# Performance work log

Measured on AMD Instinct MI355X. Metric: run time of the kernel, lower is better.

Reference implementation:

```python
import jax, jax.numpy as jnp
import numpy as np

TOP_K_PERCENT = 0.7


def setup_inputs() -> dict:
    key = jax.random.key(0)
    k1, k2, k3, k4 = jax.random.split(key, 4)
    B, C, H, W = 4, 19, 512, 1024
    logits = jax.random.normal(k1, (B, C, H, W), dtype=jnp.float32)
    labels = jax.random.randint(k2, (B, H, W), 0, C, dtype=jnp.int64)
    smooth_labels = jax.random.uniform(k3, (B, C, H, W), dtype=jnp.float32)
    weight2 = jax.random.uniform(k4, (C,), dtype=jnp.float32)
    return {"logits": logits, "labels": labels, "smooth_labels": smooth_labels, "weight2": weight2}


def reference(logits, labels, smooth_labels, weight2):
    # Fused equivalent of the per-class loop:
    #   cum[b,h,w] = sum_c smooth[b,c,h,w] * weight2[c] * (-log_softmax(logits)[b,c,h,w])
    # (ignore_label=-1 never matches any class index, so no masking occurs.)
    logp = jax.nn.log_softmax(logits, axis=1)  # [B,C,H,W]
    w = weight2[None, :, None, None]
    pixel_losses_2 = -(smooth_labels * w * logp).sum(axis=1)  # [B,H,W]
    flat = pixel_losses_2.reshape(-1)
    k = int(TOP_K_PERCENT * flat.shape[0])  # static shape -> python int
    top_vals, _ = jax.lax.top_k(flat, k)
    return top_vals.mean()
```

## Files before the change

kernel.cpp:

```cpp
#include <hip/hip_runtime.h>

#define NPIX 2097152
#define NT4  524288
#define NCH  19
#define CPL4 131072
#define KSEL 1468006u
#define LBS  1024
#define LBLK (NT4/LBS)
#define HB   512
#define NCP  8
#define H1B  4096
#define H2B  1024

#define OFF_COMB1 (NPIX*4)
#define OFF_COMB2 (OFF_COMB1 + NCP*H1B*4)
#define OFF_COMB3 (OFF_COMB2 + NCP*H2B*4)
#define OFF_TICK  (OFF_COMB3 + NCP*H2B*4)
#define OFF_PART  (OFF_TICK + 16)
#define OFF_CTRL  (OFF_PART + HB*8)
#define ZBYTES    (OFF_TICK + 16 - OFF_COMB1)

__global__ __launch_bounds__(LBS) void k_loss(
    const float* __restrict__ logits, const float* __restrict__ smooth,
    const float* __restrict__ wgt, float* __restrict__ loss,
    unsigned* __restrict__ comb1)
{
    __shared__ unsigned h[H1B];
    for (int j = threadIdx.x; j < H1B; j += LBS) h[j] = 0u;

    int tid = blockIdx.x * LBS + threadIdx.x;
    int img = tid >> 17;
    int rem = tid & (CPL4 - 1);
    const float4* L = (const float4*)logits + (size_t)img * (NCH * CPL4) + rem;
    const float4* S = (const float4*)smooth + (size_t)img * (NCH * CPL4) + rem;

    float4 xb[3], sb[3];
    #pragma unroll
    for (int i = 0; i < 3; ++i) {
        xb[i] = L[(size_t)i * CPL4];
        sb[i] = S[(size_t)i * CPL4];
    }
    __syncthreads();

    float s0 = 0.f, s1 = 0.f, s2 = 0.f, s3 = 0.f;
    float sw0 = 0.f, sw1 = 0.f, sw2 = 0.f, sw3 = 0.f;
    float swl0 = 0.f, swl1 = 0.f, swl2 = 0.f, swl3 = 0.f;

    #pragma unroll
    for (int c = 0; c < NCH; ++c) {
        float4 xv = xb[c % 3];
        float4 sv = sb[c % 3];
        if (c + 3 < NCH) {
            xb[c % 3] = L[(size_t)(c + 3) * CPL4];
            sb[c % 3] = S[(size_t)(c + 3) * CPL4];
        }
        float wc = wgt[c];
        s0 += __expf(xv.x); s1 += __expf(xv.y);
        s2 += __expf(xv.z); s3 += __expf(xv.w);
        float t0 = sv.x * wc, t1 = sv.y * wc, t2 = sv.z * wc, t3 = sv.w * wc;
        sw0 += t0; sw1 += t1; sw2 += t2; sw3 += t3;
        swl0 = fmaf(t0, xv.x, swl0); swl1 = fmaf(t1, xv.y, swl1);
        swl2 = fmaf(t2, xv.z, swl2); swl3 = fmaf(t3, xv.w, swl3);
    }

    float l0 = fmaxf(__logf(s0) * sw0 - swl0, 0.f);
    float l1 = fmaxf(__logf(s1) * sw1 - swl1, 0.f);
    float l2 = fmaxf(__logf(s2) * sw2 - swl2, 0.f);
    float l3 = fmaxf(__logf(s3) * sw3 - swl3, 0.f);
    ((float4*)loss)[tid] = make_float4(l0, l1, l2, l3);

    atomicAdd(&h[__float_as_uint(l0) >> 20], 1u);
    atomicAdd(&h[__float_as_uint(l1) >> 20], 1u);
    atomicAdd(&h[__float_as_uint(l2) >> 20], 1u);
    atomicAdd(&h[__float_as_uint(l3) >> 20], 1u);
    __syncthreads();

    unsigned* dst = comb1 + (size_t)(blockIdx.x & (NCP - 1)) * H1B;
    for (int j = threadIdx.x; j < H1B; j += LBS) {
        unsigned c = h[j];
        if (c) atomicAdd(&dst[j], c);
    }
}

__device__ __forceinline__ void suffix_select(
    unsigned* h, unsigned* cs, unsigned* shv, int cpt, unsigned need)
{
    int t = threadIdx.x;
    unsigned sum = 0;
    for (int j = 0; j < cpt; ++j) sum += h[t * cpt + j];
    cs[t] = sum;
    __syncthreads();
    for (int off = 1; off < 256; off <<= 1) {
        unsigned v = (t + off < 256) ? cs[t + off] : 0u;
        __syncthreads();
        cs[t] += v;
        __syncthreads();
    }
    unsigned St = cs[t], Sn = (t < 255) ? cs[t + 1] : 0u;
    if (St >= need && Sn < need) { shv[0] = (unsigned)t; shv[1] = Sn; }
    __syncthreads();
    if (t == 0) {
        unsigned cum = shv[1];
        for (int bb = (int)shv[0] * cpt + cpt - 1;; --bb) {
            unsigned c = h[bb];
            if (cum + c >= need) { shv[2] = (unsigned)bb; shv[3] = need - cum; break; }
            cum += c;
        }
    }
    __syncthreads();
}

#define ALD(p)  __hip_atomic_load((p), __ATOMIC_RELAXED, __HIP_MEMORY_SCOPE_AGENT)

__global__ __launch_bounds__(256) void k_h2(
    const uint4* __restrict__ lb, const unsigned* __restrict__ comb1,
    unsigned* __restrict__ comb2, unsigned* __restrict__ ctrl)
{
    __shared__ unsigned bins[H1B];
    __shared__ unsigned cs[256];
    __shared__ unsigned shv[4];
    int t = threadIdx.x, b = blockIdx.x;

    for (int j = t; j < H1B; j += 256) {
        unsigned s = 0;
        #pragma unroll
        for (int cp = 0; cp < NCP; ++cp) s += comb1[(size_t)cp * H1B + j];
        bins[j] = s;
    }
    __syncthreads();
    suffix_select(bins, cs, shv, H1B / 256, KSEL);
    unsigned p1 = shv[2], n1 = shv[3];
    if (b == 0 && t == 0) { ctrl[0] = p1; ctrl[1] = n1; }

    for (int j = t; j < H2B; j += 256) bins[j] = 0u;
    __syncthreads();
    int base = b * 256 + t;
    #pragma unroll
    for (int k = 0; k < NT4 / (HB * 256); ++k) {
        uint4 v = lb[(size_t)k * (HB * 256) + base];
        if ((v.x >> 20) == p1) atomicAdd(&bins[(v.x >> 10) & 1023u], 1u);
        if ((v.y >> 20) == p1) atomicAdd(&bins[(v.y >> 10) & 1023u], 1u);
        if ((v.z >> 20) == p1) atomicAdd(&bins[(v.z >> 10) & 1023u], 1u);
        if ((v.w >> 20) == p1) atomicAdd(&bins[(v.w >> 10) & 1023u], 1u);
    }
    __syncthreads();
    unsigned* dst = comb2 + (size_t)(b & (NCP - 1)) * H2B;
    for (int j = t; j < H2B; j += 256)
        if (bins[j]) atomicAdd(&dst[j], bins[j]);
}

__global__ __launch_bounds__(256) void k_h3(
    const uint4* __restrict__ lb, const unsigned* __restrict__ comb2,
    unsigned* __restrict__ comb3, double* __restrict__ partials,
    const unsigned* __restrict__ ctrl, unsigned* __restrict__ ticket,
    float* __restrict__ out)
{
    __shared__ unsigned bins[H2B];
    __shared__ unsigned cs[256];
    __shared__ unsigned shv[4];
    __shared__ double wsum[4];
    __shared__ unsigned sh_last;
    int t = threadIdx.x, b = blockIdx.x;
    unsigned p1 = ctrl[0], n1 = ctrl[1];

    for (int j = t; j < H2B; j += 256) {
        unsigned s = 0;
        #pragma unroll
        for (int cp = 0; cp < NCP; ++cp) s += comb2[(size_t)cp * H2B + j];
        bins[j] = s;
    }
    __syncthreads();
    suffix_select(bins, cs, shv, H2B / 256, n1);
    unsigned p2 = (p1 << 10) | shv[2], n2 = shv[3];

    for (int j = t; j < H2B; j += 256) bins[j] = 0u;
    __syncthreads();
    double acc = 0.0;
    int base = b * 256 + t;
    #pragma unroll
    for (int k = 0; k < NT4 / (HB * 256); ++k) {
        uint4 v = lb[(size_t)k * (HB * 256) + base];
        unsigned px = v.x >> 10, py = v.y >> 10, pz = v.z >> 10, pw = v.w >> 10;
        if (px == p2) atomicAdd(&bins[v.x & 1023u], 1u);
        else if (px > p2) acc += (double)__uint_as_float(v.x);
        if (py == p2) atomicAdd(&bins[v.y & 1023u], 1u);
        else if (py > p2) acc += (double)__uint_as_float(v.y);
        if (pz == p2) atomicAdd(&bins[v.z & 1023u], 1u);
        else if (pz > p2) acc += (double)__uint_as_float(v.z);
        if (pw == p2) atomicAdd(&bins[v.w & 1023u], 1u);
        else if (pw > p2) acc += (double)__uint_as_float(v.w);
    }
    __syncthreads();
    unsigned* dst = comb3 + (size_t)(b & (NCP - 1)) * H2B;
    for (int j = t; j < H2B; j += 256)
        if (bins[j]) atomicAdd(&dst[j], bins[j]);

    #pragma unroll
    for (int off = 32; off > 0; off >>= 1) acc += __shfl_down(acc, off, 64);
    if ((t & 63) == 0) wsum[t >> 6] = acc;
    __syncthreads();
    if (t == 0) {
        partials[b] = wsum[0] + wsum[1] + wsum[2] + wsum[3];
        __threadfence();
        sh_last = (atomicAdd(ticket, 1u) == HB - 1) ? 1u : 0u;
    }
    __syncthreads();
    if (!sh_last) return;

    __threadfence();
    for (int j = t; j < H2B; j += 256) {
        unsigned s = 0;
        #pragma unroll
        for (int cp = 0; cp < NCP; ++cp) s += ALD(&comb3[(size_t)cp * H2B + j]);
        bins[j] = s;
    }
    __syncthreads();
    suffix_select(bins, cs, shv, H2B / 256, n2);
    unsigned b3 = shv[2], r2 = shv[3];

    double a2 = __hip_atomic_load(&partials[t], __ATOMIC_RELAXED, __HIP_MEMORY_SCOPE_AGENT)
              + __hip_atomic_load(&partials[t + 256], __ATOMIC_RELAXED, __HIP_MEMORY_SCOPE_AGENT);
    #pragma unroll
    for (int kk = 0; kk < 4; ++kk) {
        int bb = t * 4 + kk;
        if (bb > (int)b3 && bins[bb])
            a2 += (double)bins[bb] * (double)__uint_as_float((p2 << 10) | (unsigned)bb);
    }
    #pragma unroll
    for (int off = 32; off > 0; off >>= 1) a2 += __shfl_down(a2, off, 64);
    if ((t & 63) == 0) wsum[t >> 6] = a2;
    __syncthreads();
    if (t == 0) {
        double tot = wsum[0] + wsum[1] + wsum[2] + wsum[3];
        tot += (double)r2 * (double)__uint_as_float((p2 << 10) | b3);
        out[0] = (float)(tot / (double)KSEL);
    }
}

extern "C" void kernel_launch(void* const* d_in, const int* in_sizes, int n_in,
                              void* d_out, int out_size, void* d_ws, size_t ws_size,
                              hipStream_t stream)
{
    const float* logits = (const float*)d_in[0];
    const float* smooth = (const float*)d_in[2];
    const float* wgt    = (const float*)d_in[3];

    char* ws = (char*)d_ws;
    float*    loss     = (float*)ws;
    unsigned* comb1    = (unsigned*)(ws + OFF_COMB1);
    unsigned* comb2    = (unsigned*)(ws + OFF_COMB2);
    unsigned* comb3    = (unsigned*)(ws + OFF_COMB3);
    unsigned* ticket   = (unsigned*)(ws + OFF_TICK);
    double*   partials = (double*)(ws + OFF_PART);
    unsigned* ctrl     = (unsigned*)(ws + OFF_CTRL);
    const uint4* lb    = (const uint4*)loss;

    hipMemsetAsync(ws + OFF_COMB1, 0, ZBYTES, stream);
    k_loss<<<LBLK, LBS, 0, stream>>>(logits, smooth, wgt, loss, comb1);
    k_h2  <<<HB,   256, 0, stream>>>(lb, comb1, comb2, ctrl);
    k_h3  <<<HB,   256, 0, stream>>>(lb, comb2, comb3, partials, ctrl,
                                     ticket, (float*)d_out);
}
```

Measured before the change: 361.0 us.

## Replace three-pass radix select with a 20-bit global histogram and one refinement pass

The loss kernel now bins each pixel loss into a 1M-bin global histogram (two copies) with direct global atomics, replacing the 12-bit shared-memory histogram. A new chunked-sum kernel finds the 20-bit prefix bucket containing the k-th value without rereading the loss buffer, so the second full pass over the 8 MB loss array is gone. Only one 4096-bin refinement pass remains. The trade-off is 2M global atomics spread over an 8 MB histogram that must be zeroed by the memset each call, plus heavier scans of that histogram, instead of cheap shared-memory atomics.

```diff
diff --git a/kernel.cpp b/kernel.cpp
--- a/kernel.cpp
+++ b/kernel.cpp
@@ -8,26 +8,27 @@
 #define LBS  1024
 #define LBLK (NT4/LBS)
 #define HB   512
-#define NCP  8
-#define H1B  4096
-#define H2B  1024
-
-#define OFF_COMB1 (NPIX*4)
-#define OFF_COMB2 (OFF_COMB1 + NCP*H1B*4)
-#define OFF_COMB3 (OFF_COMB2 + NCP*H2B*4)
-#define OFF_TICK  (OFF_COMB3 + NCP*H2B*4)
-#define OFF_PART  (OFF_TICK + 16)
+#define HBINS (1u<<20)
+#define NCPA 2
+#define CHUNK 2048
+#define H3B  4096
+#define NCP3 4
+
+#define OFF_COMBA (NPIX*4)
+#define OFF_COMB3 (OFF_COMBA + NCPA*HBINS*4)
+#define OFF_TICK  (OFF_COMB3 + NCP3*H3B*4)
+#define OFF_CHS   (OFF_TICK + 16)
+#define OFF_PART  (OFF_CHS + HB*4)
 #define OFF_CTRL  (OFF_PART + HB*8)
-#define ZBYTES    (OFF_TICK + 16 - OFF_COMB1)
+#define ZBYTES    (OFF_TICK + 16 - OFF_COMBA)
+
+#define ALD(p)  __hip_atomic_load((p), __ATOMIC_RELAXED, __HIP_MEMORY_SCOPE_AGENT)
 
 __global__ __launch_bounds__(LBS) void k_loss(
     const float* __restrict__ logits, const float* __restrict__ smooth,
     const float* __restrict__ wgt, float* __restrict__ loss,
-    unsigned* __restrict__ comb1)
-{
-    __shared__ unsigned h[H1B];
-    for (int j = threadIdx.x; j < H1B; j += LBS) h[j] = 0u;
-
+    unsigned* __restrict__ combA)
+{
     int tid = blockIdx.x * LBS + threadIdx.x;
     int img = tid >> 17;
     int rem = tid & (CPL4 - 1);
@@ -40,7 +41,6 @@
         xb[i] = L[(size_t)i * CPL4];
         sb[i] = S[(size_t)i * CPL4];
     }
-    __syncthreads();
 
     float s0 = 0.f, s1 = 0.f, s2 = 0.f, s3 = 0.f;
     float sw0 = 0.f, sw1 = 0.f, sw2 = 0.f, sw3 = 0.f;
@@ -69,17 +69,11 @@
     float l3 = fmaxf(__logf(s3) * sw3 - swl3, 0.f);
     ((float4*)loss)[tid] = make_float4(l0, l1, l2, l3);
 
-    atomicAdd(&h[__float_as_uint(l0) >> 20], 1u);
-    atomicAdd(&h[__float_as_uint(l1) >> 20], 1u);
-    atomicAdd(&h[__float_as_uint(l2) >> 20], 1u);
-    atomicAdd(&h[__float_as_uint(l3) >> 20], 1u);
-    __syncthreads();
-
-    unsigned* dst = comb1 + (size_t)(blockIdx.x & (NCP - 1)) * H1B;
-    for (int j = threadIdx.x; j < H1B; j += LBS) {
-        unsigned c = h[j];
-        if (c) atomicAdd(&dst[j], c);
-    }
+    unsigned* hA = combA + (size_t)(blockIdx.x & (NCPA - 1)) * HBINS;
+    atomicAdd(&hA[__float_as_uint(l0) >> 12], 1u);
+    atomicAdd(&hA[__float_as_uint(l1) >> 12], 1u);
+    atomicAdd(&hA[__float_as_uint(l2) >> 12], 1u);
+    atomicAdd(&hA[__float_as_uint(l3) >> 12], 1u);
 }
 
 __device__ __forceinline__ void suffix_select(
@@ -110,121 +104,117 @@
     __syncthreads();
 }
 
-#define ALD(p)  __hip_atomic_load((p), __ATOMIC_RELAXED, __HIP_MEMORY_SCOPE_AGENT)
-
-__global__ __launch_bounds__(256) void k_h2(
-    const uint4* __restrict__ lb, const unsigned* __restrict__ comb1,
-    unsigned* __restrict__ comb2, unsigned* __restrict__ ctrl)
-{
-    __shared__ unsigned bins[H1B];
+__global__ __launch_bounds__(256) void k_selA(
+    const unsigned* __restrict__ combA, unsigned* __restrict__ chunkS,
+    unsigned* __restrict__ tick, unsigned* __restrict__ ctrl)
+{
+    __shared__ unsigned hA[CHUNK];
     __shared__ unsigned cs[256];
     __shared__ unsigned shv[4];
+    __shared__ unsigned ws[4];
+    __shared__ unsigned sh_last;
     int t = threadIdx.x, b = blockIdx.x;
 
-    for (int j = t; j < H1B; j += 256) {
-        unsigned s = 0;
-        #pragma unroll
-        for (int cp = 0; cp < NCP; ++cp) s += comb1[(size_t)cp * H1B + j];
-        bins[j] = s;
-    }
-    __syncthreads();
-    suffix_select(bins, cs, shv, H1B / 256, KSEL);
-    unsigned p1 = shv[2], n1 = shv[3];
-    if (b == 0 && t == 0) { ctrl[0] = p1; ctrl[1] = n1; }
-
-    for (int j = t; j < H2B; j += 256) bins[j] = 0u;
-    __syncthreads();
-    int base = b * 256 + t;
-    #pragma unroll
-    for (int k = 0; k < NT4 / (HB * 256); ++k) {
-        uint4 v = lb[(size_t)k * (HB * 256) + base];
-        if ((v.x >> 20) == p1) atomicAdd(&bins[(v.x >> 10) & 1023u], 1u);
-        if ((v.y >> 20) == p1) atomicAdd(&bins[(v.y >> 10) & 1023u], 1u);
-        if ((v.z >> 20) == p1) atomicAdd(&bins[(v.z >> 10) & 1023u], 1u);
-        if ((v.w >> 20) == p1) atomicAdd(&bins[(v.w >> 10) & 1023u], 1u);
-    }
-    __syncthreads();
-    unsigned* dst = comb2 + (size_t)(b & (NCP - 1)) * H2B;
-    for (int j = t; j < H2B; j += 256)
-        if (bins[j]) atomicAdd(&dst[j], bins[j]);
-}
-
-__global__ __launch_bounds__(256) void k_h3(
-    const uint4* __restrict__ lb, const unsigned* __restrict__ comb2,
+    const uint4* c0 = (const uint4*)(combA + (size_t)b * CHUNK);
+    const uint4* c1 = (const uint4*)(combA + HBINS + (size_t)b * CHUNK);
+    unsigned s = 0;
+    #pragma unroll
+    for (int i = 0; i < CHUNK / 4 / 256; ++i) {
+        uint4 a = c0[i * 256 + t], d = c1[i * 256 + t];
+        s += a.x + a.y + a.z + a.w + d.x + d.y + d.z + d.w;
+    }
+    #pragma unroll
+    for (int off = 32; off > 0; off >>= 1) s += __shfl_down(s, off, 64);
+    if ((t & 63) == 0) ws[t >> 6] = s;
+    __syncthreads();
+    if (t == 0) {
+        chunkS[b] = ws[0] + ws[1] + ws[2] + ws[3];
+        __threadfence();
+        sh_last = (atomicAdd(&tick[0], 1u) == HB - 1) ? 1u : 0u;
+    }
+    __syncthreads();
+    if (!sh_last) return;
+    __threadfence();
+
+    for (int j = t; j < HB; j += 256) hA[j] = ALD(&chunkS[j]);
+    __syncthreads();
+    suffix_select(hA, cs, shv, HB / 256, KSEL);
+    unsigned cstar = shv[2], needp = shv[3];
+    __syncthreads();
+    for (int j = t; j < CHUNK; j += 256)
+        hA[j] = ALD(&combA[(size_t)cstar * CHUNK + j])
+              + ALD(&combA[HBINS + (size_t)cstar * CHUNK + j]);
+    __syncthreads();
+    suffix_select(hA, cs, shv, CHUNK / 256, needp);
+    if (t == 0) { ctrl[0] = cstar * CHUNK + shv[2]; ctrl[1] = shv[3]; }
+}
+
+__global__ __launch_bounds__(256) void k_h3fin(
+    const uint4* __restrict__ lb, const unsigned* __restrict__ ctrl,
     unsigned* __restrict__ comb3, double* __restrict__ partials,
-    const unsigned* __restrict__ ctrl, unsigned* __restrict__ ticket,
-    float* __restrict__ out)
-{
-    __shared__ unsigned bins[H2B];
+    unsigned* __restrict__ tick, float* __restrict__ out)
+{
+    __shared__ unsigned bins[H3B];
     __shared__ unsigned cs[256];
     __shared__ unsigned shv[4];
     __shared__ double wsum[4];
     __shared__ unsigned sh_last;
     int t = threadIdx.x, b = blockIdx.x;
-    unsigned p1 = ctrl[0], n1 = ctrl[1];
-
-    for (int j = t; j < H2B; j += 256) {
+    unsigned pA = ctrl[0], nA = ctrl[1];
+
+    for (int j = t; j < H3B; j += 256) bins[j] = 0u;
+    __syncthreads();
+    double acc = 0.0;
+    int base = b * 256 + t;
+    #pragma unroll
+    for (int k = 0; k < NT4 / (HB * 256); ++k) {
+        uint4 v = lb[(size_t)k * (HB * 256) + base];
+        unsigned px = v.x >> 12, py = v.y >> 12, pz = v.z >> 12, pw = v.w >> 12;
+        if (px == pA) atomicAdd(&bins[v.x & 4095u], 1u);
+        else if (px > pA) acc += (double)__uint_as_float(v.x);
+        if (py == pA) atomicAdd(&bins[v.y & 4095u], 1u);
+        else if (py > pA) acc += (double)__uint_as_float(v.y);
+        if (pz == pA) atomicAdd(&bins[v.z & 4095u], 1u);
+        else if (pz > pA) acc += (double)__uint_as_float(v.z);
+        if (pw == pA) atomicAdd(&bins[v.w & 4095u], 1u);
+        else if (pw > pA) acc += (double)__uint_as_float(v.w);
+    }
+    __syncthreads();
+    unsigned* dst = comb3 + (size_t)(b & (NCP3 - 1)) * H3B;
+    for (int j = t; j < H3B; j += 256)
+        if (bins[j]) atomicAdd(&dst[j], bins[j]);
+
+    #pragma unroll
+    for (int off = 32; off > 0; off >>= 1) acc += __shfl_down(acc, off, 64);
+    if ((t & 63) == 0) wsum[t >> 6] = acc;
+    __syncthreads();
+    if (t == 0) {
+        partials[b] = wsum[0] + wsum[1] + wsum[2] + wsum[3];
+        __threadfence();
+        sh_last = (atomicAdd(&tick[1], 1u) == HB - 1) ? 1u : 0u;
+    }
+    __syncthreads();
+    if (!sh_last) return;
+    __threadfence();
+
+    for (int j = t; j < H3B; j += 256) {
         unsigned s = 0;
         #pragma unroll
-        for (int cp = 0; cp < NCP; ++cp) s += comb2[(size_t)cp * H2B + j];
+        for (int cp = 0; cp < NCP3; ++cp) s += ALD(&comb3[(size_t)cp * H3B + j]);
         bins[j] = s;
     }
     __syncthreads();
-    suffix_select(bins, cs, shv, H2B / 256, n1);
-    unsigned p2 = (p1 << 10) | shv[2], n2 = shv[3];
-
-    for (int j = t; j < H2B; j += 256) bins[j] = 0u;
-    __syncthreads();
-    double acc = 0.0;
-    int base = b * 256 + t;
-    #pragma unroll
-    for (int k = 0; k < NT4 / (HB * 256); ++k) {
-        uint4 v = lb[(size_t)k * (HB * 256) + base];
-        unsigned px = v.x >> 10, py = v.y >> 10, pz = v.z >> 10, pw = v.w >> 10;
-        if (px == p2) atomicAdd(&bins[v.x & 1023u], 1u);
-        else if (px > p2) acc += (double)__uint_as_float(v.x);
-        if (py == p2) atomicAdd(&bins[v.y & 1023u], 1u);
-        else if (py > p2) acc += (double)__uint_as_float(v.y);
-        if (pz == p2) atomicAdd(&bins[v.z & 1023u], 1u);
-        else if (pz > p2) acc += (double)__uint_as_float(v.z);
-        if (pw == p2) atomicAdd(&bins[v.w & 1023u], 1u);
-        else if (pw > p2) acc += (double)__uint_as_float(v.w);
-    }
-    __syncthreads();
-    unsigned* dst = comb3 + (size_t)(b & (NCP - 1)) * H2B;
-    for (int j = t; j < H2B; j += 256)
-        if (bins[j]) atomicAdd(&dst[j], bins[j]);
-
-    #pragma unroll
-    for (int off = 32; off > 0; off >>= 1) acc += __shfl_down(acc, off, 64);
-    if ((t & 63) == 0) wsum[t >> 6] = acc;
-    __syncthreads();
-    if (t == 0) {
-        partials[b] = wsum[0] + wsum[1] + wsum[2] + wsum[3];
-        __threadfence();
-        sh_last = (atomicAdd(ticket, 1u) == HB - 1) ? 1u : 0u;
-    }
-    __syncthreads();
-    if (!sh_last) return;
-
-    __threadfence();
-    for (int j = t; j < H2B; j += 256) {
-        unsigned s = 0;
-        #pragma unroll
-        for (int cp = 0; cp < NCP; ++cp) s += ALD(&comb3[(size_t)cp * H2B + j]);
-        bins[j] = s;
-    }
-    __syncthreads();
-    suffix_select(bins, cs, shv, H2B / 256, n2);
+    suffix_select(bins, cs, shv, H3B / 256, nA);
     unsigned b3 = shv[2], r2 = shv[3];
 
-    double a2 = __hip_atomic_load(&partials[t], __ATOMIC_RELAXED, __HIP_MEMORY_SCOPE_AGENT)
-              + __hip_atomic_load(&partials[t + 256], __ATOMIC_RELAXED, __HIP_MEMORY_SCOPE_AGENT);
-    #pragma unroll
-    for (int kk = 0; kk < 4; ++kk) {
-        int bb = t * 4 + kk;
+    double a2 = ALD((const unsigned long long*)&partials[t]) * 0.0;
+    a2 = __hip_atomic_load(&partials[t], __ATOMIC_RELAXED, __HIP_MEMORY_SCOPE_AGENT)
+       + __hip_atomic_load(&partials[t + 256], __ATOMIC_RELAXED, __HIP_MEMORY_SCOPE_AGENT);
+    #pragma unroll
+    for (int kk = 0; kk < 16; ++kk) {
+        int bb = t * 16 + kk;
         if (bb > (int)b3 && bins[bb])
-            a2 += (double)bins[bb] * (double)__uint_as_float((p2 << 10) | (unsigned)bb);
+            a2 += (double)bins[bb] * (double)__uint_as_float((pA << 12) | (unsigned)bb);
     }
     #pragma unroll
     for (int off = 32; off > 0; off >>= 1) a2 += __shfl_down(a2, off, 64);
@@ -232,7 +222,7 @@
     __syncthreads();
     if (t == 0) {
         double tot = wsum[0] + wsum[1] + wsum[2] + wsum[3];
-        tot += (double)r2 * (double)__uint_as_float((p2 << 10) | b3);
+        tot += (double)r2 * (double)__uint_as_float((pA << 12) | b3);
         out[0] = (float)(tot / (double)KSEL);
     }
 }
@@ -247,17 +237,17 @@
 
     char* ws = (char*)d_ws;
     float*    loss     = (float*)ws;
-    unsigned* comb1    = (unsigned*)(ws + OFF_COMB1);
-    unsigned* comb2    = (unsigned*)(ws + OFF_COMB2);
+    unsigned* combA    = (unsigned*)(ws + OFF_COMBA);
     unsigned* comb3    = (unsigned*)(ws + OFF_COMB3);
-    unsigned* ticket   = (unsigned*)(ws + OFF_TICK);
+    unsigned* tick     = (unsigned*)(ws + OFF_TICK);
+    unsigned* chunkS   = (unsigned*)(ws + OFF_CHS);
     double*   partials = (double*)(ws + OFF_PART);
     unsigned* ctrl     = (unsigned*)(ws + OFF_CTRL);
     const uint4* lb    = (const uint4*)loss;
 
-    hipMemsetAsync(ws + OFF_COMB1, 0, ZBYTES, stream);
-    k_loss<<<LBLK, LBS, 0, stream>>>(logits, smooth, wgt, loss, comb1);
-    k_h2  <<<HB,   256, 0, stream>>>(lb, comb1, comb2, ctrl);
-    k_h3  <<<HB,   256, 0, stream>>>(lb, comb2, comb3, partials, ctrl,
-                                     ticket, (float*)d_out);
-}
+    hipMemsetAsync(ws + OFF_COMBA, 0, ZBYTES, stream);
+    k_loss <<<LBLK, LBS, 0, stream>>>(logits, smooth, wgt, loss, combA);
+    k_selA <<<HB,   256, 0, stream>>>(combA, chunkS, tick, ctrl);
+    k_h3fin<<<HB,   256, 0, stream>>>(lb, ctrl, comb3, partials, tick,
+                                      (float*)d_out);
+}
```

Result: slower. 718.3 us (+99.0%).
